# Kernel optimization log

Measured on AMD Instinct MI355X. Metric: run time of the kernel, lower is better.

## Reference

```python
import jax, jax.numpy as jnp
import numpy as np

B, D, E = 8192, 2048, 8


def setup_inputs() -> dict:
    key = jax.random.key(0)
    k1, k2, k3, k4 = jax.random.split(key, 4)
    x = jax.random.normal(k1, (B, D), dtype=jnp.float32)
    W = jax.random.normal(k2, (E, D, D), dtype=jnp.float32) * (1.0 / np.sqrt(D))
    b = jax.random.normal(k3, (E, D), dtype=jnp.float32) * 0.02
    module_indices = jax.random.randint(k4, (B,), 0, E, dtype=jnp.int64)
    return {"x": x, "W": W, "b": b, "module_indices": module_indices}


def reference(x, W, b, module_indices):
    # Each row i of x is processed by expert module_indices[i]:
    #   out[i] = x[i] @ W[e] + b[e],  e = module_indices[i]
    # Vectorized as: run every expert on every token (E dense GEMMs),
    # then select the assigned expert per token via one-hot combine.
    y_all = jnp.einsum('bd,edo->beo', x, W) + b[None, :, :]   # [B, E, D]
    onehot = jax.nn.one_hot(module_indices, W.shape[0], dtype=x.dtype)  # [B, E]
    out = jnp.einsum('beo,be->bo', y_all, onehot)             # [B, D]
    return out
```

## Files before the change

kernel.cpp:

```cpp
#include <hip/hip_runtime.h>
#include <hip/hip_bf16.h>
#include <stdint.h>


#define B_TOK 8192
#define DIM   2048
#define NEXP  8
#define BM 256
#define BN 256
#define BK 64

typedef __attribute__((ext_vector_type(4))) float f32x4;
typedef __attribute__((ext_vector_type(8))) short s16x8;

__device__ __forceinline__ uint32_t f2bf(float f) {
    uint32_t u = __float_as_uint(f);
    uint32_t r = u + 0x7fffu + ((u >> 16) & 1u);
    return r >> 16;
}

__device__ __forceinline__ void async16(const void* g, void* l) {
    __builtin_amdgcn_global_load_lds(
        (const __attribute__((address_space(1))) uint32_t*)g,
        (__attribute__((address_space(3))) uint32_t*)l, 16, 0, 0);
}

__global__ __launch_bounds__(256) void k_prep(const float* __restrict__ x,
                                              const float* __restrict__ W,
                                              const int* __restrict__ idx,
                                              int* __restrict__ meta,
                                              int* __restrict__ perm,
                                              uint16_t* __restrict__ xb,
                                              uint16_t* __restrict__ Wt) {
    __shared__ __align__(16) char smem[16640];
    int bid = blockIdx.x;
    int t = threadIdx.x;

    if (bid == 0) {
        int (*cnt)[9] = (int(*)[9])smem;
        int* offS = (int*)(smem + 9216);
        int myIdx[32];
        #pragma unroll
        for (int i = 0; i < 32; ++i) myIdx[i] = idx[t * 32 + i];
        int c[NEXP] = {0, 0, 0, 0, 0, 0, 0, 0};
        #pragma unroll
        for (int i = 0; i < 32; ++i) {
            int e = myIdx[i];
            #pragma unroll
            for (int k = 0; k < NEXP; ++k) c[k] += (e == k) ? 1 : 0;
        }
        #pragma unroll
        for (int k = 0; k < NEXP; ++k) cnt[t][k] = c[k];
        __syncthreads();
        if (t < NEXP) {
            int run = 0;
            for (int j = 0; j < 256; ++j) { int v = cnt[j][t]; cnt[j][t] = run; run += v; }
            offS[t] = run;
        }
        __syncthreads();
        if (t == 0) {
            int off = 0;
            #pragma unroll
            for (int e = 0; e < NEXP; ++e) {
                int v = offS[e];
                offS[e] = off; meta[16 + e] = off; off += v;
            }
            offS[NEXP] = off; meta[16 + NEXP] = off;
        }
        __syncthreads();
        int base[NEXP];
        #pragma unroll
        for (int k = 0; k < NEXP; ++k) base[k] = offS[k] + cnt[t][k];
        #pragma unroll
        for (int i = 0; i < 32; ++i) {
            int e = myIdx[i];
            int pos = 0;
            #pragma unroll
            for (int k = 0; k < NEXP; ++k) pos += (e == k) ? base[k] : 0;
            perm[pos] = t * 32 + i;
            #pragma unroll
            for (int k = 0; k < NEXP; ++k) base[k] += (e == k) ? 1 : 0;
        }
        return;
    }

    if (bid <= B_TOK) {
        int p = bid - 1;
        const float4* xin = (const float4*)(x + (size_t)p * DIM);
        float4 a = xin[2 * t];
        float4 c = xin[2 * t + 1];
        uint4 o;
        o.x = f2bf(a.x) | (f2bf(a.y) << 16);
        o.y = f2bf(a.z) | (f2bf(a.w) << 16);
        o.z = f2bf(c.x) | (f2bf(c.y) << 16);
        o.w = f2bf(c.z) | (f2bf(c.w) << 16);
        *(uint4*)(xb + (size_t)p * DIM + t * 8) = o;
        return;
    }

    int wb = bid - (B_TOK + 1);
    int bx = wb & 15, by = (wb >> 4) & 31, e = wb >> 9;
    int d0 = bx * 128, o0 = by * 64;
    uint32_t (*lds)[65] = (uint32_t(*)[65])smem;
    const float* Wp = W + ((size_t)e * DIM + d0) * DIM + o0;
    #pragma unroll
    for (int p = 0; p < 4; ++p) {
        int dp = p * 16 + (t >> 4);
        int oc = (t & 15) * 4;
        const float* r0 = Wp + (size_t)(2 * dp) * DIM + oc;
        float4 v0 = *(const float4*)r0;
        float4 v1 = *(const float4*)(r0 + DIM);
        lds[oc + 0][dp ^ (((oc + 0) & 15) << 2)] = f2bf(v0.x) | (f2bf(v1.x) << 16);
        lds[oc + 1][dp ^ (((oc + 1) & 15) << 2)] = f2bf(v0.y) | (f2bf(v1.y) << 16);
        lds[oc + 2][dp ^ (((oc + 2) & 15) << 2)] = f2bf(v0.z) | (f2bf(v1.z) << 16);
        lds[oc + 3][dp ^ (((oc + 3) & 15) << 2)] = f2bf(v0.w) | (f2bf(v1.w) << 16);
    }
    __syncthreads();
    uint16_t* Wo = Wt + ((size_t)e * DIM + o0) * DIM + d0;
    #pragma unroll
    for (int q = 0; q < 4; ++q) {
        int o = q * 16 + (t >> 4);
        int cb = ((t & 15) * 4) ^ ((o & 15) << 2);
        uint4 w = *(const uint4*)&lds[o][cb];
        *(uint4*)(Wo + (size_t)o * DIM + (t & 15) * 8) = w;
    }
}

__global__ __launch_bounds__(512, 2) void k_gemm(
    const uint16_t* __restrict__ xb, const uint16_t* __restrict__ Wt,
    const float* __restrict__ bias, const int* __restrict__ meta,
    const int* __restrict__ perm, float* __restrict__ out) {
    __shared__ uint16_t As[2][BM * BK];
    __shared__ uint16_t Bs[2][BN * BK];
    __shared__ int permS[BM];

    int id = blockIdx.y;
    int e = -1, seg0 = 0, segc = 0;
    for (int i = 0; i < NEXP; ++i) {
        int o0 = meta[16 + i], o1 = meta[16 + i + 1];
        int tiles = (o1 - o0 + BM - 1) / BM;
        if (id < tiles) { e = i; seg0 = o0; segc = o1 - o0; break; }
        id -= tiles;
    }
    if (e < 0) return;
    int m0 = seg0 + id * BM;
    int valid = segc - id * BM; if (valid > BM) valid = BM;
    int n0 = blockIdx.x * BN;

    int tid = threadIdx.x;
    if (tid < BM) permS[tid] = (tid < valid) ? perm[m0 + tid] : 0;

    int wave = tid >> 6, lane = tid & 63;
    int wm = (wave >> 2) * 128, wn = (wave & 3) * 64;
    int lr = lane & 15, quad = lane >> 4;

    const uint16_t* aSrc[4];
    const uint16_t* bSrc[4];
    #pragma unroll
    for (int c = 0; c < 4; ++c) {
        int ch = c * 512 + tid;
        int row = ch >> 3;
        int kc = ((ch & 7) ^ (row & 7)) * 8;
        int pr = m0 + row; if (pr > B_TOK - 1) pr = B_TOK - 1;
        aSrc[c] = xb + (size_t)perm[pr] * DIM + kc;
        bSrc[c] = Wt + ((size_t)e * DIM + n0 + row) * DIM + kc;
    }

    auto STAGE = [&](int buf, int k0) {
        #pragma unroll
        for (int c = 0; c < 4; ++c) {
            int ch = c * 512 + tid;
            async16(aSrc[c] + k0, &As[buf][ch * 8]);
            async16(bSrc[c] + k0, &Bs[buf][ch * 8]);
        }
    };

    f32x4 acc[8][4] = {};
    STAGE(0, 0);
    __syncthreads();

    int cur = 0;
    int sw = lr & 7;
    for (int k0 = 0; k0 < DIM; k0 += BK) {
        if (k0 + BK < DIM) STAGE(cur ^ 1, k0 + BK);
        #pragma unroll
        for (int s = 0; s < 2; ++s) {
            s16x8 af[8], bfr[4];
            #pragma unroll
            for (int i = 0; i < 8; ++i)
                af[i] = *(const s16x8*)&As[cur][(wm + i * 16 + lr) * BK + (((s * 4 + quad) ^ sw) * 8)];
            #pragma unroll
            for (int j = 0; j < 4; ++j)
                bfr[j] = *(const s16x8*)&Bs[cur][(wn + j * 16 + lr) * BK + (((s * 4 + quad) ^ sw) * 8)];
            #pragma unroll
            for (int i = 0; i < 8; ++i)
                #pragma unroll
                for (int j = 0; j < 4; ++j)
                    acc[i][j] = __builtin_amdgcn_mfma_f32_16x16x32_bf16(af[i], bfr[j], acc[i][j], 0, 0, 0);
        }
        __syncthreads();
        cur ^= 1;
    }

    #pragma unroll
    for (int j = 0; j < 4; ++j) {
        int col = n0 + wn + j * 16 + lr;
        float bv = bias[e * DIM + col];
        #pragma unroll
        for (int i = 0; i < 8; ++i) {
            #pragma unroll
            for (int r = 0; r < 4; ++r) {
                int lrow = wm + i * 16 + quad * 4 + r;
                if (lrow < valid) {
                    out[(size_t)permS[lrow] * DIM + col] = acc[i][j][r] + bv;
                }
            }
        }
    }
}

extern "C" void kernel_launch(void* const* d_in, const int* in_sizes, int n_in,
                              void* d_out, int out_size, void* d_ws, size_t ws_size,
                              hipStream_t stream) {
    const float* x    = (const float*)d_in[0];
    const float* W    = (const float*)d_in[1];
    const float* bias = (const float*)d_in[2];
    const int*   idx  = (const int*)d_in[3];
    float* out = (float*)d_out;

    char* ws = (char*)d_ws;
    int* meta = (int*)ws;
    int* perm = (int*)(ws + 256);
    uint16_t* xb = (uint16_t*)(ws + 65536);
    uint16_t* Wt = (uint16_t*)(ws + 65536 + (size_t)B_TOK * DIM * 2);

    k_prep<<<1 + B_TOK + 4096, 256, 0, stream>>>(x, W, idx, meta, perm, xb, Wt);
    k_gemm<<<dim3(DIM / BN, B_TOK / BM + NEXP, 1), 512, 0, stream>>>(
        xb, Wt, bias, meta, perm, out);
}
```

Baseline: 436.3 us.

## Pipeline GEMM K-loop in half-tiles with fine-grained waitcnt and tile remapping

Restructures the grouped GEMM main loop so each 64-wide K tile is split into two 32-wide halves, staged asynchronously in a rolling schedule with explicit vmcnt waits and barriers. The aim is to overlap global-to-LDS loads with MFMA work more tightly, and s_setprio is raised around the MFMA bursts. Full tiles and partial tail tiles are now separated, with a templated path that skips MFMAs for empty rows. Blocks are launched on a flat 1D grid with an interleaved mapping across experts. The hand-written waitcnt counts and barriers are fragile and add synchronisation points per sub-step.

```diff
diff --git a/kernel.cpp b/kernel.cpp
--- a/kernel.cpp
+++ b/kernel.cpp
@@ -126,26 +126,12 @@
     }
 }
 
-__global__ __launch_bounds__(512, 2) void k_gemm(
+template<bool FULL>
+__device__ __forceinline__ void gemm_core(
+    uint16_t (*As)[2][8192], uint16_t (*Bs)[2][8192], int* permS,
     const uint16_t* __restrict__ xb, const uint16_t* __restrict__ Wt,
-    const float* __restrict__ bias, const int* __restrict__ meta,
-    const int* __restrict__ perm, float* __restrict__ out) {
-    __shared__ uint16_t As[2][BM * BK];
-    __shared__ uint16_t Bs[2][BN * BK];
-    __shared__ int permS[BM];
-
-    int id = blockIdx.y;
-    int e = -1, seg0 = 0, segc = 0;
-    for (int i = 0; i < NEXP; ++i) {
-        int o0 = meta[16 + i], o1 = meta[16 + i + 1];
-        int tiles = (o1 - o0 + BM - 1) / BM;
-        if (id < tiles) { e = i; seg0 = o0; segc = o1 - o0; break; }
-        id -= tiles;
-    }
-    if (e < 0) return;
-    int m0 = seg0 + id * BM;
-    int valid = segc - id * BM; if (valid > BM) valid = BM;
-    int n0 = blockIdx.x * BN;
+    const float* __restrict__ bias, const int* __restrict__ perm,
+    float* __restrict__ out, int e, int m0, int valid, int n0) {
 
     int tid = threadIdx.x;
     if (tid < BM) permS[tid] = (tid < valid) ? perm[m0 + tid] : 0;
@@ -153,54 +139,88 @@
     int wave = tid >> 6, lane = tid & 63;
     int wm = (wave >> 2) * 128, wn = (wave & 3) * 64;
     int lr = lane & 15, quad = lane >> 4;
-
-    const uint16_t* aSrc[4];
-    const uint16_t* bSrc[4];
-    #pragma unroll
-    for (int c = 0; c < 4; ++c) {
-        int ch = c * 512 + tid;
-        int row = ch >> 3;
-        int kc = ((ch & 7) ^ (row & 7)) * 8;
-        int pr = m0 + row; if (pr > B_TOK - 1) pr = B_TOK - 1;
-        aSrc[c] = xb + (size_t)perm[pr] * DIM + kc;
-        bSrc[c] = Wt + ((size_t)e * DIM + n0 + row) * DIM + kc;
-    }
-
-    auto STAGE = [&](int buf, int k0) {
-        #pragma unroll
-        for (int c = 0; c < 4; ++c) {
-            int ch = c * 512 + tid;
-            async16(aSrc[c] + k0, &As[buf][ch * 8]);
-            async16(bSrc[c] + k0, &Bs[buf][ch * 8]);
-        }
+    const int rdswz = (quad ^ ((lr >> 1) & 3)) * 8;
+    int nfw = 8;
+    if (!FULL) { nfw = (valid > wm) ? ((valid - wm + 15) >> 4) : 0; if (nfw > 8) nfw = 8; }
+
+    const int srcswz = (((tid & 3) ^ ((tid >> 3) & 3)) * 8);
+    const uint16_t* aPtr[2];
+    const uint16_t* bPtr[2];
+    #pragma unroll
+    for (int c = 0; c < 2; ++c) {
+        int row = c * 128 + (tid >> 2);
+        int ar = m0 + row; if (ar > B_TOK - 1) ar = B_TOK - 1;
+        aPtr[c] = xb + (size_t)perm[ar] * DIM + srcswz;
+        bPtr[c] = Wt + ((size_t)e * DIM + n0 + row) * DIM + srcswz;
+    }
+
+    auto stageA = [&](int buf, int h, int koff) {
+        #pragma unroll
+        for (int c = 0; c < 2; ++c)
+            async16(aPtr[c] + koff, &As[buf][h][(c * 512 + tid) * 8]);
     };
+    auto stageB = [&](int buf, int h, int koff) {
+        #pragma unroll
+        for (int c = 0; c < 2; ++c)
+            async16(bPtr[c] + koff, &Bs[buf][h][(c * 512 + tid) * 8]);
+    };
 
     f32x4 acc[8][4] = {};
-    STAGE(0, 0);
-    __syncthreads();
-
-    int cur = 0;
-    int sw = lr & 7;
-    for (int k0 = 0; k0 < DIM; k0 += BK) {
-        if (k0 + BK < DIM) STAGE(cur ^ 1, k0 + BK);
-        #pragma unroll
-        for (int s = 0; s < 2; ++s) {
-            s16x8 af[8], bfr[4];
-            #pragma unroll
-            for (int i = 0; i < 8; ++i)
-                af[i] = *(const s16x8*)&As[cur][(wm + i * 16 + lr) * BK + (((s * 4 + quad) ^ sw) * 8)];
-            #pragma unroll
-            for (int j = 0; j < 4; ++j)
-                bfr[j] = *(const s16x8*)&Bs[cur][(wn + j * 16 + lr) * BK + (((s * 4 + quad) ^ sw) * 8)];
-            #pragma unroll
-            for (int i = 0; i < 8; ++i)
+
+    stageA(0, 0, 0);  stageB(0, 0, 0);
+    stageA(0, 1, 32); stageB(0, 1, 32);
+    stageA(1, 0, 64); stageB(1, 0, 64);
+    asm volatile("s_waitcnt vmcnt(8)" ::: "memory");
+    __builtin_amdgcn_s_barrier();
+
+    for (int it = 0; it < DIM / 128; ++it) {
+        int t0 = 2 * it;
+        #pragma unroll
+        for (int tp = 0; tp < 2; ++tp) {
+            s16x8 bfr[4];
+            #pragma unroll
+            for (int q = 0; q < 4; ++q) {
+                const int p = tp * 4 + q;
+                const int fh = q & 1, ks = q >> 1;
+                if (p & 1) asm volatile("s_waitcnt vmcnt(6)" ::: "memory");
+                s16x8 af[4];
                 #pragma unroll
-                for (int j = 0; j < 4; ++j)
-                    acc[i][j] = __builtin_amdgcn_mfma_f32_16x16x32_bf16(af[i], bfr[j], acc[i][j], 0, 0, 0);
-        }
-        __syncthreads();
-        cur ^= 1;
-    }
+                for (int ii = 0; ii < 4; ++ii)
+                    af[ii] = *(const s16x8*)&As[tp][ks][(wm + (fh * 4 + ii) * 16 + lr) * 32 + rdswz];
+                if (fh == 0) {
+                    #pragma unroll
+                    for (int j = 0; j < 4; ++j)
+                        bfr[j] = *(const s16x8*)&Bs[tp][ks][(wn + j * 16 + lr) * 32 + rdswz];
+                }
+                {
+                    int koff = (p == 0 || p == 1) ? (t0 + 1) * 64 + 32
+                             : (p == 2 || p == 3) ? (t0 + 2) * 64
+                             : (p == 4 || p == 5) ? (t0 + 2) * 64 + 32
+                                                  : (t0 + 3) * 64;
+                    if (koff > DIM - 32) koff = DIM - 32;
+                    const int sb = (p <= 1 || p >= 6) ? 1 : 0;
+                    const int sh = (p <= 1 || p == 4 || p == 5) ? 1 : 0;
+                    if ((p & 1) == 0) stageA(sb, sh, koff);
+                    else              stageB(sb, sh, koff);
+                }
+                __builtin_amdgcn_s_barrier();
+                asm volatile("s_waitcnt lgkmcnt(0)" ::: "memory");
+                __builtin_amdgcn_s_setprio(1);
+                #pragma unroll
+                for (int ii = 0; ii < 4; ++ii) {
+                    if (FULL || (fh * 4 + ii) < nfw) {
+                        #pragma unroll
+                        for (int j = 0; j < 4; ++j)
+                            acc[fh * 4 + ii][j] = __builtin_amdgcn_mfma_f32_16x16x32_bf16(
+                                af[ii], bfr[j], acc[fh * 4 + ii][j], 0, 0, 0);
+                    }
+                }
+                __builtin_amdgcn_s_setprio(0);
+                __builtin_amdgcn_s_barrier();
+            }
+        }
+    }
+    asm volatile("s_waitcnt vmcnt(0)" ::: "memory");
 
     #pragma unroll
     for (int j = 0; j < 4; ++j) {
@@ -217,6 +237,51 @@
             }
         }
     }
+}
+
+__global__ __launch_bounds__(512, 2) void k_gemm(
+    const uint16_t* __restrict__ xb, const uint16_t* __restrict__ Wt,
+    const float* __restrict__ bias, const int* __restrict__ meta,
+    const int* __restrict__ perm, float* __restrict__ out) {
+    __shared__ uint16_t As[2][2][8192];
+    __shared__ uint16_t Bs[2][2][8192];
+    __shared__ int permS[BM];
+
+    int nf[NEXP], s0e[NEXP];
+    int F = 0;
+    #pragma unroll
+    for (int i = 0; i < NEXP; ++i) {
+        s0e[i] = meta[16 + i];
+        int c = meta[17 + i] - s0e[i];
+        nf[i] = c >> 8;
+        F += nf[i];
+    }
+    int b = blockIdx.x;
+    int e = 0, m0 = 0, valid = 0, bx = 0;
+    if (b < F * 8) {
+        int g = (b & 7) * F + (b >> 3);
+        int yf = g >> 3; bx = g & 7;
+        int a = 0;
+        #pragma unroll
+        for (int i = 0; i < NEXP; ++i) {
+            if (yf >= a && yf < a + nf[i]) { e = i; m0 = s0e[i] + (yf - a) * BM; }
+            a += nf[i];
+        }
+        valid = BM;
+    } else {
+        int pi = b - F * 8;
+        int pe = pi >> 3; bx = pi & 7;
+        if (pe >= NEXP) return;
+        int c = meta[17 + pe] - meta[16 + pe];
+        int rem = c - ((c >> 8) << 8);
+        if (rem == 0) return;
+        e = pe; m0 = s0e[pe] + (c >> 8) * BM; valid = rem;
+    }
+    int n0 = bx * BN;
+    if (valid == BM)
+        gemm_core<true >(As, Bs, permS, xb, Wt, bias, perm, out, e, m0, BM,    n0);
+    else
+        gemm_core<false>(As, Bs, permS, xb, Wt, bias, perm, out, e, m0, valid, n0);
 }
 
 extern "C" void kernel_launch(void* const* d_in, const int* in_sizes, int n_in,
@@ -235,6 +300,5 @@
     uint16_t* Wt = (uint16_t*)(ws + 65536 + (size_t)B_TOK * DIM * 2);
 
     k_prep<<<1 + B_TOK + 4096, 256, 0, stream>>>(x, W, idx, meta, perm, xb, Wt);
-    k_gemm<<<dim3(DIM / BN, B_TOK / BM + NEXP, 1), 512, 0, stream>>>(
-        xb, Wt, bias, meta, perm, out);
-}
+    k_gemm<<<320, 512, 0, stream>>>(xb, Wt, bias, meta, perm, out);
+}
```

After: 397.8 us. -8.8%, faster.

## Shrink GEMM tiles to 128x128x32 with 1D grid remap and partial-tile MFMA skipping

Applied to the files above, without the earlier changes.

Cuts the grouped GEMM tile from 256x256x64 to 128x128x32 so each 512-thread block keeps far fewer accumulators and can fit four blocks per CU. The 2D grid becomes a flat 1152-block launch, with blocks remapped in groups of eight, presumably so neighbouring blocks land on different XCDs. The expert segment search is unrolled. A templated core skips MFMAs for unused 16-row fragments in partial tiles. The smaller tiles raise the number of global loads per FLOP and double the number of k-iterations, each of which ends in a barrier.

```diff
diff --git a/kernel.cpp b/kernel.cpp
--- a/kernel.cpp
+++ b/kernel.cpp
@@ -6,9 +6,9 @@
 #define B_TOK 8192
 #define DIM   2048
 #define NEXP  8
-#define BM 256
-#define BN 256
-#define BK 64
+#define BM 128
+#define BN 128
+#define BK 32
 
 typedef __attribute__((ext_vector_type(4))) float f32x4;
 typedef __attribute__((ext_vector_type(8))) short s16x8;
@@ -126,7 +126,80 @@
     }
 }
 
-__global__ __launch_bounds__(512, 2) void k_gemm(
+template<bool FULL>
+__device__ __forceinline__ void gemm_core(
+    uint16_t (*As)[BM * BK], uint16_t (*Bs)[BN * BK], int* permS,
+    const uint16_t* __restrict__ xb, const uint16_t* __restrict__ Wt,
+    const float* __restrict__ bias, const int* __restrict__ perm,
+    float* __restrict__ out, int e, int m0, int valid, int n0) {
+
+    int tid = threadIdx.x;
+    if (tid < BM) permS[tid] = (tid < valid) ? perm[m0 + tid] : 0;
+
+    int wave = tid >> 6, lane = tid & 63;
+    int wm = (wave >> 2) * 64;
+    int wn = (wave & 3) * 32;
+    int lr = lane & 15, quad = lane >> 4;
+    const int rdswz = (quad ^ (lr & 3)) * 8;
+    int nfw = 4;
+    if (!FULL) { nfw = (valid > wm) ? ((valid - wm + 15) >> 4) : 0; if (nfw > 4) nfw = 4; }
+
+    const int srcswz = (((tid & 3) ^ ((tid >> 2) & 3)) * 8);
+    int arow = m0 + (tid >> 2); if (arow > B_TOK - 1) arow = B_TOK - 1;
+    const uint16_t* aSrc = xb + (size_t)perm[arow] * DIM + srcswz;
+    const uint16_t* bSrc = Wt + ((size_t)e * DIM + n0 + (tid >> 2)) * DIM + srcswz;
+
+    auto STAGE = [&](int buf, int k0) {
+        async16(aSrc + k0, &As[buf][tid * 8]);
+        async16(bSrc + k0, &Bs[buf][tid * 8]);
+    };
+
+    f32x4 acc[4][2] = {};
+
+    STAGE(0, 0);
+    __syncthreads();
+
+    int cur = 0;
+    for (int k0 = 0; k0 < DIM; k0 += BK) {
+        if (k0 + BK < DIM) STAGE(cur ^ 1, k0 + BK);
+        s16x8 af[4], bf[2];
+        #pragma unroll
+        for (int ii = 0; ii < 4; ++ii)
+            af[ii] = *(const s16x8*)&As[cur][(wm + ii * 16 + lr) * BK + rdswz];
+        #pragma unroll
+        for (int j = 0; j < 2; ++j)
+            bf[j] = *(const s16x8*)&Bs[cur][(wn + j * 16 + lr) * BK + rdswz];
+        #pragma unroll
+        for (int ii = 0; ii < 4; ++ii) {
+            if (FULL || ii < nfw) {
+                #pragma unroll
+                for (int j = 0; j < 2; ++j)
+                    acc[ii][j] = __builtin_amdgcn_mfma_f32_16x16x32_bf16(
+                        af[ii], bf[j], acc[ii][j], 0, 0, 0);
+            }
+        }
+        __syncthreads();
+        cur ^= 1;
+    }
+
+    #pragma unroll
+    for (int j = 0; j < 2; ++j) {
+        int col = n0 + wn + j * 16 + lr;
+        float bv = bias[e * DIM + col];
+        #pragma unroll
+        for (int ii = 0; ii < 4; ++ii) {
+            #pragma unroll
+            for (int r = 0; r < 4; ++r) {
+                int lrow = wm + ii * 16 + quad * 4 + r;
+                if (lrow < valid) {
+                    out[(size_t)permS[lrow] * DIM + col] = acc[ii][j][r] + bv;
+                }
+            }
+        }
+    }
+}
+
+__global__ __launch_bounds__(512, 4) void k_gemm(
     const uint16_t* __restrict__ xb, const uint16_t* __restrict__ Wt,
     const float* __restrict__ bias, const int* __restrict__ meta,
     const int* __restrict__ perm, float* __restrict__ out) {
@@ -134,89 +207,30 @@
     __shared__ uint16_t Bs[2][BN * BK];
     __shared__ int permS[BM];
 
-    int id = blockIdx.y;
-    int e = -1, seg0 = 0, segc = 0;
+    int b = blockIdx.x;
+    int g = (b & 7) * 144 + (b >> 3);
+    int yf = g >> 4, bx = g & 15;
+
+    int e = -1, mloc = 0, cnt = 0, s0 = 0;
+    int a = 0;
+    #pragma unroll
     for (int i = 0; i < NEXP; ++i) {
-        int o0 = meta[16 + i], o1 = meta[16 + i + 1];
-        int tiles = (o1 - o0 + BM - 1) / BM;
-        if (id < tiles) { e = i; seg0 = o0; segc = o1 - o0; break; }
-        id -= tiles;
+        int ci = meta[17 + i] - meta[16 + i];
+        int nfi = (ci + 127) >> 7;
+        if (e < 0 && yf >= a && yf < a + nfi) {
+            e = i; mloc = yf - a; cnt = ci; s0 = meta[16 + i];
+        }
+        a += nfi;
     }
     if (e < 0) return;
-    int m0 = seg0 + id * BM;
-    int valid = segc - id * BM; if (valid > BM) valid = BM;
-    int n0 = blockIdx.x * BN;
-
-    int tid = threadIdx.x;
-    if (tid < BM) permS[tid] = (tid < valid) ? perm[m0 + tid] : 0;
-
-    int wave = tid >> 6, lane = tid & 63;
-    int wm = (wave >> 2) * 128, wn = (wave & 3) * 64;
-    int lr = lane & 15, quad = lane >> 4;
-
-    const uint16_t* aSrc[4];
-    const uint16_t* bSrc[4];
-    #pragma unroll
-    for (int c = 0; c < 4; ++c) {
-        int ch = c * 512 + tid;
-        int row = ch >> 3;
-        int kc = ((ch & 7) ^ (row & 7)) * 8;
-        int pr = m0 + row; if (pr > B_TOK - 1) pr = B_TOK - 1;
-        aSrc[c] = xb + (size_t)perm[pr] * DIM + kc;
-        bSrc[c] = Wt + ((size_t)e * DIM + n0 + row) * DIM + kc;
-    }
-
-    auto STAGE = [&](int buf, int k0) {
-        #pragma unroll
-        for (int c = 0; c < 4; ++c) {
-            int ch = c * 512 + tid;
-            async16(aSrc[c] + k0, &As[buf][ch * 8]);
-            async16(bSrc[c] + k0, &Bs[buf][ch * 8]);
-        }
-    };
-
-    f32x4 acc[8][4] = {};
-    STAGE(0, 0);
-    __syncthreads();
-
-    int cur = 0;
-    int sw = lr & 7;
-    for (int k0 = 0; k0 < DIM; k0 += BK) {
-        if (k0 + BK < DIM) STAGE(cur ^ 1, k0 + BK);
-        #pragma unroll
-        for (int s = 0; s < 2; ++s) {
-            s16x8 af[8], bfr[4];
-            #pragma unroll
-            for (int i = 0; i < 8; ++i)
-                af[i] = *(const s16x8*)&As[cur][(wm + i * 16 + lr) * BK + (((s * 4 + quad) ^ sw) * 8)];
-            #pragma unroll
-            for (int j = 0; j < 4; ++j)
-                bfr[j] = *(const s16x8*)&Bs[cur][(wn + j * 16 + lr) * BK + (((s * 4 + quad) ^ sw) * 8)];
-            #pragma unroll
-            for (int i = 0; i < 8; ++i)
-                #pragma unroll
-                for (int j = 0; j < 4; ++j)
-                    acc[i][j] = __builtin_amdgcn_mfma_f32_16x16x32_bf16(af[i], bfr[j], acc[i][j], 0, 0, 0);
-        }
-        __syncthreads();
-        cur ^= 1;
-    }
-
-    #pragma unroll
-    for (int j = 0; j < 4; ++j) {
-        int col = n0 + wn + j * 16 + lr;
-        float bv = bias[e * DIM + col];
-        #pragma unroll
-        for (int i = 0; i < 8; ++i) {
-            #pragma unroll
-            for (int r = 0; r < 4; ++r) {
-                int lrow = wm + i * 16 + quad * 4 + r;
-                if (lrow < valid) {
-                    out[(size_t)permS[lrow] * DIM + col] = acc[i][j][r] + bv;
-                }
-            }
-        }
-    }
+    int m0 = s0 + mloc * BM;
+    int valid = cnt - mloc * BM; if (valid > BM) valid = BM;
+    int n0 = bx * BN;
+
+    if (valid == BM)
+        gemm_core<true >(As, Bs, permS, xb, Wt, bias, perm, out, e, m0, BM,    n0);
+    else
+        gemm_core<false>(As, Bs, permS, xb, Wt, bias, perm, out, e, m0, valid, n0);
 }
 
 extern "C" void kernel_launch(void* const* d_in, const int* in_sizes, int n_in,
@@ -235,6 +249,5 @@
     uint16_t* Wt = (uint16_t*)(ws + 65536 + (size_t)B_TOK * DIM * 2);
 
     k_prep<<<1 + B_TOK + 4096, 256, 0, stream>>>(x, W, idx, meta, perm, xb, Wt);
-    k_gemm<<<dim3(DIM / BN, B_TOK / BM + NEXP, 1), 512, 0, stream>>>(
-        xb, Wt, bias, meta, perm, out);
-}
+    k_gemm<<<1152, 512, 0, stream>>>(xb, Wt, bias, meta, perm, out);
+}
```

Result: no change. 431.9 us (-1.0%).
